# Kernel tuning notes

Hardware: AMD Instinct MI355X
Metric: run time of the kernel (lower is better)

The kernel has to match this reference:

```python
import jax, jax.numpy as jnp
import numpy as np
from jax import lax

N_TRACES = 128
TRACE_LEN = 32          # uniform trace length -> seq_len
INPUT_DIM = 64
HIDDEN_DIM = 128
BATCH = N_TRACES * TRACE_LEN  # 4096 events = batch_size


def setup_inputs() -> dict:
    key = jax.random.key(0)
    ks = jax.random.split(key, 12)
    s = 1.0 / np.sqrt(HIDDEN_DIM)
    u = lambda k, shape: jax.random.uniform(k, shape, jnp.float32, -s, s)
    return {
        "input": jax.random.normal(ks[0], (BATCH, INPUT_DIM), jnp.float32),
        # layer 0 LSTM params (gate order i,f,g,o as in torch)
        "W_ih0": u(ks[1], (4 * HIDDEN_DIM, INPUT_DIM)),
        "W_hh0": u(ks[2], (4 * HIDDEN_DIM, HIDDEN_DIM)),
        "b_ih0": u(ks[3], (4 * HIDDEN_DIM,)),
        "b_hh0": u(ks[4], (4 * HIDDEN_DIM,)),
        # layer 1 LSTM params
        "W_ih1": u(ks[5], (4 * HIDDEN_DIM, HIDDEN_DIM)),
        "W_hh1": u(ks[6], (4 * HIDDEN_DIM, HIDDEN_DIM)),
        "b_ih1": u(ks[7], (4 * HIDDEN_DIM,)),
        "b_hh1": u(ks[8], (4 * HIDDEN_DIM,)),
        # final linear: hidden -> 1
        "W_lin": u(ks[9], (1, HIDDEN_DIM)),
        "b_lin": u(ks[10], (1,)),
    }


def _lstm_layer(xs, W_ih, W_hh, b_ih, b_hh):
    # xs: [T, B, D_in] time-major. Returns hidden stream [T, B, H].
    H = W_hh.shape[1]
    B = xs.shape[1]
    # precompute input projection for all timesteps
    x_proj = jnp.einsum('tbd,gd->tbg', xs, W_ih) + b_ih + b_hh  # [T,B,4H]

    def step(carry, xp):
        h, c = carry
        gates = xp + h @ W_hh.T                # [B,4H]
        i, f, g, o = jnp.split(gates, 4, axis=-1)
        i = jax.nn.sigmoid(i)
        f = jax.nn.sigmoid(f)
        g = jnp.tanh(g)
        o = jax.nn.sigmoid(o)
        c = f * c + i * g
        h = o * jnp.tanh(c)
        return (h, c), h

    h0 = jnp.zeros((B, H), xs.dtype)
    _, hs = lax.scan(step, (h0, h0), x_proj)
    return hs


def _forward(input, W_ih0, W_hh0, b_ih0, b_hh0, W_ih1, W_hh1, b_ih1, b_hh1, W_lin, b_lin):
    L, D = TRACE_LEN, INPUT_DIM
    # Prefix scatter: event k of a trace gets the padded prefix events[0..k].
    x_tr = input.reshape(N_TRACES, L, D)                       # [Ntr, L, D]
    causal = (jnp.arange(L)[None, :] <= jnp.arange(L)[:, None])  # [k, j] mask j<=k
    padded = x_tr[:, None, :, :] * causal[None, :, :, None].astype(input.dtype)  # [Ntr,L(k),L(j),D]
    padded = padded.reshape(BATCH, L, D)                       # batch-first padded sequences

    xs = jnp.transpose(padded, (1, 0, 2))                      # [L, B, D] time-major
    h1 = _lstm_layer(xs, W_ih0, W_hh0, b_ih0, b_hh0)           # [L, B, H]
    h2 = _lstm_layer(h1, W_ih1, W_hh1, b_ih1, b_hh1)           # [L, B, H]

    out = jnp.einsum('tbh,oh->tbo', h2, W_lin) + b_lin         # [L, B, 1]
    # last valid timestep gather: lengths[i]-1 = (i mod L)
    lens_m1 = jnp.tile(jnp.arange(L), N_TRACES)                # [B]
    y_pred = out[lens_m1, jnp.arange(BATCH), 0]                # [B]
    return y_pred


def reference(input, W_ih0, W_hh0, b_ih0, b_hh0, W_ih1, W_hh1, b_ih1, b_hh1, W_lin, b_lin):
    return _forward(input, W_ih0, W_hh0, b_ih0, b_hh0, W_ih1, W_hh1, b_ih1, b_hh1, W_lin, b_lin)
```

## Files before the change

### kernel.cpp

```cpp
#include <hip/hip_runtime.h>

#define N_TRACES 128
#define TLEN 32
#define IN_DIM 64
#define HID 128
#define G4 (4 * HID)
#define BATCH (N_TRACES * TLEN)


__device__ __forceinline__ float fast_sigmoid(float x) {
    return 1.0f / (1.0f + __expf(-x));
}
__device__ __forceinline__ float fast_tanh(float x) {
    return 1.0f - 2.0f / (__expf(2.0f * x) + 1.0f);
}
__device__ __forceinline__ float quad_reduce(float x) {
    x += __int_as_float(__builtin_amdgcn_update_dpp(
        0, __float_as_int(x), 0xB1 , 0xF, 0xF, true));
    x += __int_as_float(__builtin_amdgcn_update_dpp(
        0, __float_as_int(x), 0x4E , 0xF, 0xF, true));
    return x;
}

__device__ __forceinline__ void load_w(const float* __restrict__ W, int u, int s,
                                       float (&w)[4][32]) {
    #pragma unroll
    for (int i = 0; i < 4; ++i) {
        const float* wr = W + (size_t)(u + 128 * i) * HID + 32 * s;
        #pragma unroll
        for (int j = 0; j < 8; ++j) {
            float4 v = *(const float4*)(wr + 4 * j);
            w[i][4 * j + 0] = v.x; w[i][4 * j + 1] = v.y;
            w[i][4 * j + 2] = v.z; w[i][4 * j + 3] = v.w;
        }
    }
    #pragma unroll
    for (int i = 0; i < 4; ++i)
        #pragma unroll
        for (int j = 0; j < 32; ++j)
            asm volatile("" : "+v"(w[i][j]));
}

__device__ __forceinline__ void matvec_acc(const float (&w)[4][32],
                                           const float* hb, float (&acc)[4]) {
    #pragma unroll
    for (int j = 0; j < 8; ++j) {
        float4 v = *(const float4*)(hb + 4 * j);
        float hx[4] = {v.x, v.y, v.z, v.w};
        #pragma unroll
        for (int e = 0; e < 4; ++e) {
            #pragma unroll
            for (int i = 0; i < 4; ++i)
                acc[i] = fmaf(w[i][4 * j + e], hx[e], acc[i]);
        }
    }
}


template <int K>
__global__ __launch_bounds__(256) void gemm_bt(
    const float* __restrict__ A,
    const float* __restrict__ W,
    const float* __restrict__ b1,
    const float* __restrict__ b2,
    float* __restrict__ out,
    int Nld)
{
    constexpr int LD = 68;
    __shared__ float At[K][LD];
    __shared__ float Wt[K][LD];

    const int tid = threadIdx.x;
    const int m0 = blockIdx.x * 64;
    const int n0 = blockIdx.y * 64;

    const int rot = tid & 3;
    #pragma unroll
    for (int j = 0; j < K / 16; ++j) {
        const int e = 4 * (tid + 256 * j);
        const int row = e / K;
        const int k = e % K;
        float4 va = *(const float4*)(A + (size_t)(m0 + row) * K + k);
        float4 vw = *(const float4*)(W + (size_t)(n0 + row) * K + k);
        float fa[4] = {va.x, va.y, va.z, va.w};
        float fw[4] = {vw.x, vw.y, vw.z, vw.w};
        #pragma unroll
        for (int ii = 0; ii < 4; ++ii) {
            const int i = (ii + rot) & 3;
            At[k + i][row] = fa[i];
            Wt[k + i][row] = fw[i];
        }
    }
    __syncthreads();

    const int tx = tid & 15;
    const int ty = tid >> 4;
    float acc[4][4] = {};

    #pragma unroll 4
    for (int k = 0; k < K; ++k) {
        float4 a = *(const float4*)&At[k][ty * 4];
        float4 w = *(const float4*)&Wt[k][tx * 4];
        acc[0][0] = fmaf(a.x, w.x, acc[0][0]); acc[0][1] = fmaf(a.x, w.y, acc[0][1]);
        acc[0][2] = fmaf(a.x, w.z, acc[0][2]); acc[0][3] = fmaf(a.x, w.w, acc[0][3]);
        acc[1][0] = fmaf(a.y, w.x, acc[1][0]); acc[1][1] = fmaf(a.y, w.y, acc[1][1]);
        acc[1][2] = fmaf(a.y, w.z, acc[1][2]); acc[1][3] = fmaf(a.y, w.w, acc[1][3]);
        acc[2][0] = fmaf(a.z, w.x, acc[2][0]); acc[2][1] = fmaf(a.z, w.y, acc[2][1]);
        acc[2][2] = fmaf(a.z, w.z, acc[2][2]); acc[2][3] = fmaf(a.z, w.w, acc[2][3]);
        acc[3][0] = fmaf(a.w, w.x, acc[3][0]); acc[3][1] = fmaf(a.w, w.y, acc[3][1]);
        acc[3][2] = fmaf(a.w, w.z, acc[3][2]); acc[3][3] = fmaf(a.w, w.w, acc[3][3]);
    }

    float bb[4];
    #pragma unroll
    for (int j = 0; j < 4; ++j) {
        const int n = n0 + tx * 4 + j;
        bb[j] = b1[n] + b2[n];
    }
    #pragma unroll
    for (int i = 0; i < 4; ++i) {
        const int m = m0 + ty * 4 + i;
        float4 v;
        v.x = acc[i][0] + bb[0]; v.y = acc[i][1] + bb[1];
        v.z = acc[i][2] + bb[2]; v.w = acc[i][3] + bb[3];
        *(float4*)(out + (size_t)m * Nld + n0 + tx * 4) = v;
    }
}


__global__ __launch_bounds__(512) void fused_trace(
    const float* __restrict__ xproj0,
    const float* __restrict__ Whh0,
    const float* __restrict__ Wih1,
    const float* __restrict__ bih1,
    const float* __restrict__ bhh1,
    const float* __restrict__ Whh1,
    const float* __restrict__ Wlin,
    const float* __restrict__ blin,
    float* __restrict__ y)
{
    const int trace = blockIdx.x;
    const int tid = threadIdx.x;
    const int u = tid >> 2;
    const int s = tid & 3;
    const int pu = u + 4 * (u >> 5);

    __shared__ float hs[TLEN][140];
    __shared__ float xp[TLEN * G4];

    float w[4][32];

    const float* xpb = xproj0 + (size_t)trace * TLEN * G4;
    #pragma unroll
    for (int j = 0; j < 8; ++j) {
        const int f4 = j * 512 + tid;
        float4 v = *(const float4*)(xpb + 4 * f4);
        *(float4*)(&xp[4 * f4]) = v;
    }
    load_w(Whh0, u, s, w);
    __syncthreads();

    float xg[4], xgn[4];
    #pragma unroll
    for (int i = 0; i < 4; ++i) xg[i] = xp[128 * i + u];
    #pragma unroll
    for (int i = 0; i < 4; ++i) xgn[i] = xp[G4 + 128 * i + u];

    float c = 0.0f;
    if (s == 0) {
        const float iv = fast_sigmoid(xg[0]);
        const float fv = fast_sigmoid(xg[1]);
        const float gv = fast_tanh(xg[2]);
        const float ov = fast_sigmoid(xg[3]);
        c = fv * c + iv * gv;
        hs[0][pu] = ov * fast_tanh(c);
    }
    __syncthreads();

    #pragma unroll 1
    for (int t = 1; t < TLEN; ++t) {
        #pragma unroll
        for (int i = 0; i < 4; ++i) xg[i] = xgn[i];

        float acc[4] = {0.f, 0.f, 0.f, 0.f};
        matvec_acc(w, &hs[t - 1][36 * s], acc);
        #pragma unroll
        for (int i = 0; i < 4; ++i) acc[i] = quad_reduce(acc[i]);

        if (s == 0) {
            const float iv = fast_sigmoid(acc[0] + xg[0]);
            const float fv = fast_sigmoid(acc[1] + xg[1]);
            const float gv = fast_tanh(acc[2] + xg[2]);
            const float ov = fast_sigmoid(acc[3] + xg[3]);
            c = fv * c + iv * gv;
            hs[t][pu] = ov * fast_tanh(c);
        }
        if (t < TLEN - 1) {
            #pragma unroll
            for (int i = 0; i < 4; ++i)
                xgn[i] = xp[(t + 1) * G4 + 128 * i + u];
        }
        __syncthreads();
    }

    load_w(Wih1, u, s, w);
    float bi[4] = {0.f, 0.f, 0.f, 0.f};
    if (s == 0) {
        #pragma unroll
        for (int i = 0; i < 4; ++i) bi[i] = bih1[u + 128 * i] + bhh1[u + 128 * i];
    }
    #pragma unroll 1
    for (int t = 0; t < TLEN; ++t) {
        float acc[4] = {0.f, 0.f, 0.f, 0.f};
        matvec_acc(w, &hs[t][36 * s], acc);
        #pragma unroll
        for (int i = 0; i < 4; ++i) acc[i] = quad_reduce(acc[i]);
        if (s == 0) {
            #pragma unroll
            for (int i = 0; i < 4; ++i) xp[t * G4 + 128 * i + u] = acc[i] + bi[i];
        }
    }
    __syncthreads();

    load_w(Whh1, u, s, w);
    #pragma unroll
    for (int i = 0; i < 4; ++i) xg[i] = xp[128 * i + u];
    #pragma unroll
    for (int i = 0; i < 4; ++i) xgn[i] = xp[G4 + 128 * i + u];

    c = 0.0f;
    if (s == 0) {
        const float iv = fast_sigmoid(xg[0]);
        const float fv = fast_sigmoid(xg[1]);
        const float gv = fast_tanh(xg[2]);
        const float ov = fast_sigmoid(xg[3]);
        c = fv * c + iv * gv;
        hs[0][pu] = ov * fast_tanh(c);
    }
    __syncthreads();

    #pragma unroll 1
    for (int t = 1; t < TLEN; ++t) {
        #pragma unroll
        for (int i = 0; i < 4; ++i) xg[i] = xgn[i];

        float acc[4] = {0.f, 0.f, 0.f, 0.f};
        matvec_acc(w, &hs[t - 1][36 * s], acc);
        #pragma unroll
        for (int i = 0; i < 4; ++i) acc[i] = quad_reduce(acc[i]);

        if (s == 0) {
            const float iv = fast_sigmoid(acc[0] + xg[0]);
            const float fv = fast_sigmoid(acc[1] + xg[1]);
            const float gv = fast_tanh(acc[2] + xg[2]);
            const float ov = fast_sigmoid(acc[3] + xg[3]);
            c = fv * c + iv * gv;
            hs[t][pu] = ov * fast_tanh(c);
        }
        if (t < TLEN - 1) {
            #pragma unroll
            for (int i = 0; i < 4; ++i)
                xgn[i] = xp[(t + 1) * G4 + 128 * i + u];
        }
        __syncthreads();
    }

    if (tid < 128) {
        const int tq = tid >> 2;
        const int sq = tid & 3;
        float wl[32];
        #pragma unroll
        for (int j = 0; j < 8; ++j) {
            float4 v = *(const float4*)(Wlin + 32 * sq + 4 * j);
            wl[4 * j + 0] = v.x; wl[4 * j + 1] = v.y;
            wl[4 * j + 2] = v.z; wl[4 * j + 3] = v.w;
        }
        const float* hb = &hs[tq][36 * sq];
        float a = 0.f;
        #pragma unroll
        for (int j = 0; j < 8; ++j) {
            float4 v = *(const float4*)(hb + 4 * j);
            a = fmaf(v.x, wl[4 * j + 0], a);
            a = fmaf(v.y, wl[4 * j + 1], a);
            a = fmaf(v.z, wl[4 * j + 2], a);
            a = fmaf(v.w, wl[4 * j + 3], a);
        }
        a = quad_reduce(a);
        if (sq == 0) y[trace * TLEN + tq] = a + blin[0];
    }
}


extern "C" void kernel_launch(void* const* d_in, const int* in_sizes, int n_in,
                              void* d_out, int out_size, void* d_ws, size_t ws_size,
                              hipStream_t stream) {
    const float* input = (const float*)d_in[0];
    const float* W_ih0 = (const float*)d_in[1];
    const float* W_hh0 = (const float*)d_in[2];
    const float* b_ih0 = (const float*)d_in[3];
    const float* b_hh0 = (const float*)d_in[4];
    const float* W_ih1 = (const float*)d_in[5];
    const float* W_hh1 = (const float*)d_in[6];
    const float* b_ih1 = (const float*)d_in[7];
    const float* b_hh1 = (const float*)d_in[8];
    const float* W_lin = (const float*)d_in[9];
    const float* b_lin = (const float*)d_in[10];
    float* out = (float*)d_out;

    float* xproj0 = (float*)d_ws;

    dim3 ggrid(BATCH / 64, G4 / 64);

    gemm_bt<IN_DIM><<<ggrid, 256, 0, stream>>>(input, W_ih0, b_ih0, b_hh0, xproj0, G4);
    fused_trace<<<N_TRACES, 512, 0, stream>>>(xproj0, W_hh0, W_ih1, b_ih1, b_hh1,
                                              W_hh1, W_lin, b_lin, out);
}
```

Before: 165.3 us.

## Assign two hidden units per thread and halve the fused LSTM block size

The fused per-trace LSTM kernel now gives each thread two hidden units and holds two sets of weight rows in registers (256 floats). The block shrinks from 512 to 256 threads with launch bounds (256,1). Each shared-memory h load now feeds twice as many FMAs, and fewer waves take part in each per-timestep barrier. In exchange, register pressure roughly doubles, which risks spills, and each SIMD has fewer waves to hide latency in the serial recurrence.

```diff
diff --git a/kernel.cpp b/kernel.cpp
--- a/kernel.cpp
+++ b/kernel.cpp
@@ -21,28 +21,42 @@
         0, __float_as_int(x), 0x4E , 0xF, 0xF, true));
     return x;
 }
-
-__device__ __forceinline__ void load_w(const float* __restrict__ W, int u, int s,
-                                       float (&w)[4][32]) {
-    #pragma unroll
-    for (int i = 0; i < 4; ++i) {
-        const float* wr = W + (size_t)(u + 128 * i) * HID + 32 * s;
-        #pragma unroll
-        for (int j = 0; j < 8; ++j) {
-            float4 v = *(const float4*)(wr + 4 * j);
-            w[i][4 * j + 0] = v.x; w[i][4 * j + 1] = v.y;
-            w[i][4 * j + 2] = v.z; w[i][4 * j + 3] = v.w;
-        }
-    }
-    #pragma unroll
-    for (int i = 0; i < 4; ++i)
-        #pragma unroll
-        for (int j = 0; j < 32; ++j)
-            asm volatile("" : "+v"(w[i][j]));
-}
-
-__device__ __forceinline__ void matvec_acc(const float (&w)[4][32],
-                                           const float* hb, float (&acc)[4]) {
+__device__ __forceinline__ float lstm_gate(const float (&acc)[4], const float (&xg)[4],
+                                           float& c) {
+    const float iv = fast_sigmoid(acc[0] + xg[0]);
+    const float fv = fast_sigmoid(acc[1] + xg[1]);
+    const float gv = fast_tanh(acc[2] + xg[2]);
+    const float ov = fast_sigmoid(acc[3] + xg[3]);
+    c = fv * c + iv * gv;
+    return ov * fast_tanh(c);
+}
+
+__device__ __forceinline__ void load_w2(const float* __restrict__ W, int u0, int s,
+                                        float (&w)[2][4][32]) {
+    #pragma unroll
+    for (int jj = 0; jj < 2; ++jj) {
+        #pragma unroll
+        for (int i = 0; i < 4; ++i) {
+            const float* wr = W + (size_t)(u0 + jj + 128 * i) * HID + 32 * s;
+            #pragma unroll
+            for (int j = 0; j < 8; ++j) {
+                float4 v = *(const float4*)(wr + 4 * j);
+                w[jj][i][4 * j + 0] = v.x; w[jj][i][4 * j + 1] = v.y;
+                w[jj][i][4 * j + 2] = v.z; w[jj][i][4 * j + 3] = v.w;
+            }
+        }
+    }
+    #pragma unroll
+    for (int jj = 0; jj < 2; ++jj)
+        #pragma unroll
+        for (int i = 0; i < 4; ++i)
+            #pragma unroll
+            for (int j = 0; j < 32; ++j)
+                asm volatile("" : "+v"(w[jj][i][j]));
+}
+
+__device__ __forceinline__ void matvec2(const float (&w)[2][4][32],
+                                        const float* hb, float (&acc)[2][4]) {
     #pragma unroll
     for (int j = 0; j < 8; ++j) {
         float4 v = *(const float4*)(hb + 4 * j);
@@ -50,8 +64,10 @@
         #pragma unroll
         for (int e = 0; e < 4; ++e) {
             #pragma unroll
-            for (int i = 0; i < 4; ++i)
-                acc[i] = fmaf(w[i][4 * j + e], hx[e], acc[i]);
+            for (int jj = 0; jj < 2; ++jj)
+                #pragma unroll
+                for (int i = 0; i < 4; ++i)
+                    acc[jj][i] = fmaf(w[jj][i][4 * j + e], hx[e], acc[jj][i]);
         }
     }
 }
@@ -128,7 +144,7 @@
 }
 
 
-__global__ __launch_bounds__(512) void fused_trace(
+__global__ __launch_bounds__(256, 1) void fused_trace(
     const float* __restrict__ xproj0,
     const float* __restrict__ Whh0,
     const float* __restrict__ Wih1,
@@ -141,126 +157,141 @@
 {
     const int trace = blockIdx.x;
     const int tid = threadIdx.x;
-    const int u = tid >> 2;
+    const int up = tid >> 2;
     const int s = tid & 3;
-    const int pu = u + 4 * (u >> 5);
+    const int u0 = 2 * up;
+    const int pu = u0 + 4 * (u0 >> 5);
 
     __shared__ float hs[TLEN][140];
     __shared__ float xp[TLEN * G4];
 
-    float w[4][32];
+    float w[2][4][32];
 
     const float* xpb = xproj0 + (size_t)trace * TLEN * G4;
     #pragma unroll
-    for (int j = 0; j < 8; ++j) {
-        const int f4 = j * 512 + tid;
+    for (int j = 0; j < 16; ++j) {
+        const int f4 = j * 256 + tid;
         float4 v = *(const float4*)(xpb + 4 * f4);
         *(float4*)(&xp[4 * f4]) = v;
     }
-    load_w(Whh0, u, s, w);
-    __syncthreads();
-
-    float xg[4], xgn[4];
-    #pragma unroll
-    for (int i = 0; i < 4; ++i) xg[i] = xp[128 * i + u];
-    #pragma unroll
-    for (int i = 0; i < 4; ++i) xgn[i] = xp[G4 + 128 * i + u];
-
-    float c = 0.0f;
+    load_w2(Whh0, u0, s, w);
+    __syncthreads();
+
+    float xg[2][4], xgn[2][4];
+    #pragma unroll
+    for (int jj = 0; jj < 2; ++jj)
+        #pragma unroll
+        for (int i = 0; i < 4; ++i) xg[jj][i] = xp[128 * i + u0 + jj];
+    #pragma unroll
+    for (int jj = 0; jj < 2; ++jj)
+        #pragma unroll
+        for (int i = 0; i < 4; ++i) xgn[jj][i] = xp[G4 + 128 * i + u0 + jj];
+
+    float c0 = 0.0f, c1 = 0.0f;
     if (s == 0) {
-        const float iv = fast_sigmoid(xg[0]);
-        const float fv = fast_sigmoid(xg[1]);
-        const float gv = fast_tanh(xg[2]);
-        const float ov = fast_sigmoid(xg[3]);
-        c = fv * c + iv * gv;
-        hs[0][pu] = ov * fast_tanh(c);
+        const float za[4] = {0.f, 0.f, 0.f, 0.f};
+        hs[0][pu]     = lstm_gate(za, xg[0], c0);
+        hs[0][pu + 1] = lstm_gate(za, xg[1], c1);
     }
     __syncthreads();
 
     #pragma unroll 1
     for (int t = 1; t < TLEN; ++t) {
         #pragma unroll
-        for (int i = 0; i < 4; ++i) xg[i] = xgn[i];
-
-        float acc[4] = {0.f, 0.f, 0.f, 0.f};
-        matvec_acc(w, &hs[t - 1][36 * s], acc);
-        #pragma unroll
-        for (int i = 0; i < 4; ++i) acc[i] = quad_reduce(acc[i]);
+        for (int jj = 0; jj < 2; ++jj)
+            #pragma unroll
+            for (int i = 0; i < 4; ++i) xg[jj][i] = xgn[jj][i];
+
+        float acc[2][4] = {};
+        matvec2(w, &hs[t - 1][36 * s], acc);
+        #pragma unroll
+        for (int jj = 0; jj < 2; ++jj)
+            #pragma unroll
+            for (int i = 0; i < 4; ++i) acc[jj][i] = quad_reduce(acc[jj][i]);
 
         if (s == 0) {
-            const float iv = fast_sigmoid(acc[0] + xg[0]);
-            const float fv = fast_sigmoid(acc[1] + xg[1]);
-            const float gv = fast_tanh(acc[2] + xg[2]);
-            const float ov = fast_sigmoid(acc[3] + xg[3]);
-            c = fv * c + iv * gv;
-            hs[t][pu] = ov * fast_tanh(c);
+            hs[t][pu]     = lstm_gate(acc[0], xg[0], c0);
+            hs[t][pu + 1] = lstm_gate(acc[1], xg[1], c1);
         }
         if (t < TLEN - 1) {
             #pragma unroll
+            for (int jj = 0; jj < 2; ++jj)
+                #pragma unroll
+                for (int i = 0; i < 4; ++i)
+                    xgn[jj][i] = xp[(t + 1) * G4 + 128 * i + u0 + jj];
+        }
+        __syncthreads();
+    }
+
+    load_w2(Wih1, u0, s, w);
+    float bi[2][4] = {};
+    if (s == 0) {
+        #pragma unroll
+        for (int jj = 0; jj < 2; ++jj)
+            #pragma unroll
             for (int i = 0; i < 4; ++i)
-                xgn[i] = xp[(t + 1) * G4 + 128 * i + u];
-        }
-        __syncthreads();
-    }
-
-    load_w(Wih1, u, s, w);
-    float bi[4] = {0.f, 0.f, 0.f, 0.f};
-    if (s == 0) {
-        #pragma unroll
-        for (int i = 0; i < 4; ++i) bi[i] = bih1[u + 128 * i] + bhh1[u + 128 * i];
+                bi[jj][i] = bih1[u0 + jj + 128 * i] + bhh1[u0 + jj + 128 * i];
     }
     #pragma unroll 1
     for (int t = 0; t < TLEN; ++t) {
-        float acc[4] = {0.f, 0.f, 0.f, 0.f};
-        matvec_acc(w, &hs[t][36 * s], acc);
-        #pragma unroll
-        for (int i = 0; i < 4; ++i) acc[i] = quad_reduce(acc[i]);
+        float acc[2][4] = {};
+        matvec2(w, &hs[t][36 * s], acc);
+        #pragma unroll
+        for (int jj = 0; jj < 2; ++jj)
+            #pragma unroll
+            for (int i = 0; i < 4; ++i) acc[jj][i] = quad_reduce(acc[jj][i]);
         if (s == 0) {
             #pragma unroll
-            for (int i = 0; i < 4; ++i) xp[t * G4 + 128 * i + u] = acc[i] + bi[i];
-        }
-    }
-    __syncthreads();
-
-    load_w(Whh1, u, s, w);
-    #pragma unroll
-    for (int i = 0; i < 4; ++i) xg[i] = xp[128 * i + u];
-    #pragma unroll
-    for (int i = 0; i < 4; ++i) xgn[i] = xp[G4 + 128 * i + u];
-
-    c = 0.0f;
+            for (int jj = 0; jj < 2; ++jj)
+                #pragma unroll
+                for (int i = 0; i < 4; ++i)
+                    xp[t * G4 + 128 * i + u0 + jj] = acc[jj][i] + bi[jj][i];
+        }
+    }
+    __syncthreads();
+
+    load_w2(Whh1, u0, s, w);
+    #pragma unroll
+    for (int jj = 0; jj < 2; ++jj)
+        #pragma unroll
+        for (int i = 0; i < 4; ++i) xg[jj][i] = xp[128 * i + u0 + jj];
+    #pragma unroll
+    for (int jj = 0; jj < 2; ++jj)
+        #pragma unroll
+        for (int i = 0; i < 4; ++i) xgn[jj][i] = xp[G4 + 128 * i + u0 + jj];
+
+    c0 = 0.0f; c1 = 0.0f;
     if (s == 0) {
-        const float iv = fast_sigmoid(xg[0]);
-        const float fv = fast_sigmoid(xg[1]);
-        const float gv = fast_tanh(xg[2]);
-        const float ov = fast_sigmoid(xg[3]);
-        c = fv * c + iv * gv;
-        hs[0][pu] = ov * fast_tanh(c);
+        const float za[4] = {0.f, 0.f, 0.f, 0.f};
+        hs[0][pu]     = lstm_gate(za, xg[0], c0);
+        hs[0][pu + 1] = lstm_gate(za, xg[1], c1);
     }
     __syncthreads();
 
     #pragma unroll 1
     for (int t = 1; t < TLEN; ++t) {
         #pragma unroll
-        for (int i = 0; i < 4; ++i) xg[i] = xgn[i];
-
-        float acc[4] = {0.f, 0.f, 0.f, 0.f};
-        matvec_acc(w, &hs[t - 1][36 * s], acc);
-        #pragma unroll
-        for (int i = 0; i < 4; ++i) acc[i] = quad_reduce(acc[i]);
+        for (int jj = 0; jj < 2; ++jj)
+            #pragma unroll
+            for (int i = 0; i < 4; ++i) xg[jj][i] = xgn[jj][i];
+
+        float acc[2][4] = {};
+        matvec2(w, &hs[t - 1][36 * s], acc);
+        #pragma unroll
+        for (int jj = 0; jj < 2; ++jj)
+            #pragma unroll
+            for (int i = 0; i < 4; ++i) acc[jj][i] = quad_reduce(acc[jj][i]);
 
         if (s == 0) {
-            const float iv = fast_sigmoid(acc[0] + xg[0]);
-            const float fv = fast_sigmoid(acc[1] + xg[1]);
-            const float gv = fast_tanh(acc[2] + xg[2]);
-            const float ov = fast_sigmoid(acc[3] + xg[3]);
-            c = fv * c + iv * gv;
-            hs[t][pu] = ov * fast_tanh(c);
+            hs[t][pu]     = lstm_gate(acc[0], xg[0], c0);
+            hs[t][pu + 1] = lstm_gate(acc[1], xg[1], c1);
         }
         if (t < TLEN - 1) {
             #pragma unroll
-            for (int i = 0; i < 4; ++i)
-                xgn[i] = xp[(t + 1) * G4 + 128 * i + u];
+            for (int jj = 0; jj < 2; ++jj)
+                #pragma unroll
+                for (int i = 0; i < 4; ++i)
+                    xgn[jj][i] = xp[(t + 1) * G4 + 128 * i + u0 + jj];
         }
         __syncthreads();
     }
@@ -312,6 +343,6 @@
     dim3 ggrid(BATCH / 64, G4 / 64);
 
     gemm_bt<IN_DIM><<<ggrid, 256, 0, stream>>>(input, W_ih0, b_ih0, b_hh0, xproj0, G4);
-    fused_trace<<<N_TRACES, 512, 0, stream>>>(xproj0, W_hh0, W_ih1, b_ih1, b_hh1,
+    fused_trace<<<N_TRACES, 256, 0, stream>>>(xproj0, W_hh0, W_ih1, b_ih1, b_hh1,
                                               W_hh1, W_lin, b_lin, out);
 }
```

New measurement: 201.4 us. +21.8%, slower.

## Compute layer-1 input projection with split-bf16 MFMA instead of per-step FMA matvec

Applied to the files above, without the earlier changes.

The layer-1 input projection over all 32 timesteps is moved from a per-timestep scalar FMA matvec with quad reductions onto MFMA 16x16x32 bf16 instructions. Both the hidden states and W_ih1 are split into high and low bf16 parts, and three MFMA products are summed to keep close to fp32 accuracy. This removes 32 sequential matvec iterations and their DPP reductions, replacing them with a batched tile matmul. In exchange it adds bf16 conversion work and carries a small precision risk from the split-bf16 approximation.

```diff
diff --git a/kernel.cpp b/kernel.cpp
--- a/kernel.cpp
+++ b/kernel.cpp
@@ -7,6 +7,9 @@
 #define G4 (4 * HID)
 #define BATCH (N_TRACES * TLEN)
 
+typedef float f32x4 __attribute__((ext_vector_type(4)));
+typedef __bf16 bf16x8 __attribute__((ext_vector_type(8)));
+
 
 __device__ __forceinline__ float fast_sigmoid(float x) {
     return 1.0f / (1.0f + __expf(-x));
@@ -52,6 +55,47 @@
             #pragma unroll
             for (int i = 0; i < 4; ++i)
                 acc[i] = fmaf(w[i][4 * j + e], hx[e], acc[i]);
+        }
+    }
+}
+
+
+__device__ __forceinline__ void load_wfrag(const float* __restrict__ W, int u, int q,
+                                           bf16x8 (&bh)[4][4], bf16x8 (&bl)[4][4])
+{
+    #pragma unroll
+    for (int gi = 0; gi < 4; ++gi) {
+        const float* wr = W + (size_t)(u + 128 * gi) * HID + 8 * q;
+        #pragma unroll
+        for (int kc = 0; kc < 4; ++kc) {
+            float4 v0 = *(const float4*)(wr + 32 * kc);
+            float4 v1 = *(const float4*)(wr + 32 * kc + 4);
+            float f0[4] = {v0.x, v0.y, v0.z, v0.w};
+            float f1[4] = {v1.x, v1.y, v1.z, v1.w};
+            bf16x8 h, l;
+            #pragma unroll
+            for (int e = 0; e < 4; ++e) {
+                __bf16 t0 = (__bf16)f0[e];
+                h[e] = t0; l[e] = (__bf16)(f0[e] - (float)t0);
+                __bf16 t1 = (__bf16)f1[e];
+                h[4 + e] = t1; l[4 + e] = (__bf16)(f1[e] - (float)t1);
+            }
+            bh[gi][kc] = h; bl[gi][kc] = l;
+        }
+    }
+}
+
+__device__ __forceinline__ void mm3(const bf16x8 (&ah)[4], const bf16x8 (&al)[4],
+                                    const bf16x8 (&bh)[4][4], const bf16x8 (&bl)[4][4],
+                                    f32x4 (&acc)[4])
+{
+    #pragma unroll
+    for (int gi = 0; gi < 4; ++gi) {
+        #pragma unroll
+        for (int kc = 0; kc < 4; ++kc) {
+            acc[gi] = __builtin_amdgcn_mfma_f32_16x16x32_bf16(ah[kc], bh[gi][kc], acc[gi], 0, 0, 0);
+            acc[gi] = __builtin_amdgcn_mfma_f32_16x16x32_bf16(al[kc], bh[gi][kc], acc[gi], 0, 0, 0);
+            acc[gi] = __builtin_amdgcn_mfma_f32_16x16x32_bf16(ah[kc], bl[gi][kc], acc[gi], 0, 0, 0);
         }
     }
 }
@@ -203,21 +247,49 @@
         __syncthreads();
     }
 
-    load_w(Wih1, u, s, w);
-    float bi[4] = {0.f, 0.f, 0.f, 0.f};
-    if (s == 0) {
-        #pragma unroll
-        for (int i = 0; i < 4; ++i) bi[i] = bih1[u + 128 * i] + bhh1[u + 128 * i];
-    }
-    #pragma unroll 1
-    for (int t = 0; t < TLEN; ++t) {
-        float acc[4] = {0.f, 0.f, 0.f, 0.f};
-        matvec_acc(w, &hs[t][36 * s], acc);
-        #pragma unroll
-        for (int i = 0; i < 4; ++i) acc[i] = quad_reduce(acc[i]);
-        if (s == 0) {
-            #pragma unroll
-            for (int i = 0; i < 4; ++i) xp[t * G4 + 128 * i + u] = acc[i] + bi[i];
+    {
+        const int w8 = tid >> 6;
+        const int lane = tid & 63;
+        const int cl = lane & 15;
+        const int q = lane >> 4;
+        const int um = 16 * w8 + cl;
+
+        bf16x8 Bh[4][4], Bl[4][4];
+        load_wfrag(Wih1, um, q, Bh, Bl);
+        float bim[4];
+        #pragma unroll
+        for (int gi = 0; gi < 4; ++gi)
+            bim[gi] = bih1[um + 128 * gi] + bhh1[um + 128 * gi];
+
+        #pragma unroll
+        for (int mt = 0; mt < 2; ++mt) {
+            bf16x8 ah[4], al[4];
+            #pragma unroll
+            for (int kc = 0; kc < 4; ++kc) {
+                const float* ph = &hs[16 * mt + cl][36 * kc + 8 * q];
+                float4 v0 = *(const float4*)(ph);
+                float4 v1 = *(const float4*)(ph + 4);
+                float f0[4] = {v0.x, v0.y, v0.z, v0.w};
+                float f1[4] = {v1.x, v1.y, v1.z, v1.w};
+                bf16x8 hh, ll;
+                #pragma unroll
+                for (int e = 0; e < 4; ++e) {
+                    __bf16 t0 = (__bf16)f0[e];
+                    hh[e] = t0; ll[e] = (__bf16)(f0[e] - (float)t0);
+                    __bf16 t1 = (__bf16)f1[e];
+                    hh[4 + e] = t1; ll[4 + e] = (__bf16)(f1[e] - (float)t1);
+                }
+                ah[kc] = hh; al[kc] = ll;
+            }
+            f32x4 acc[4];
+            #pragma unroll
+            for (int gi = 0; gi < 4; ++gi) acc[gi] = (f32x4){0.f, 0.f, 0.f, 0.f};
+            mm3(ah, al, Bh, Bl, acc);
+            #pragma unroll
+            for (int gi = 0; gi < 4; ++gi)
+                #pragma unroll
+                for (int r = 0; r < 4; ++r)
+                    xp[(16 * mt + 4 * q + r) * G4 + 128 * gi + um] = acc[gi][r] + bim[gi];
         }
     }
     __syncthreads();
```

After: 153.4 us. 1.08x faster.
